# Kernel optimization log

Hardware: AMD Instinct MI355X
Metric: run time of the kernel (lower is better)

The kernel has to match this reference:

```python
import jax, jax.numpy as jnp
import numpy as np

B, Q, K = 4, 512, 512
QUERY_SIZE = 512
KEY_SIZE = 512
NUM_HIDDENS = 256


def setup_inputs() -> dict:
    key = jax.random.key(0)
    k1, k2, k3, k4, k5 = jax.random.split(key, 5)
    queries = jax.random.normal(k1, (B, Q, 1, QUERY_SIZE), dtype=jnp.float32)
    keys = jax.random.normal(k2, (B, 1, K, KEY_SIZE), dtype=jnp.float32)
    # nn.Linear weights (bias=False); stored as (in, out) for einsum clarity
    W_q = jax.random.normal(k3, (QUERY_SIZE, NUM_HIDDENS), dtype=jnp.float32) * (1.0 / np.sqrt(QUERY_SIZE))
    W_k = jax.random.normal(k4, (KEY_SIZE, NUM_HIDDENS), dtype=jnp.float32) * (1.0 / np.sqrt(KEY_SIZE))
    w_v = jax.random.normal(k5, (NUM_HIDDENS,), dtype=jnp.float32) * (1.0 / np.sqrt(NUM_HIDDENS))
    return {"queries": queries, "keys": keys, "W_q": W_q, "W_k": W_k, "w_v": w_v}


def reference(queries, keys, W_q, W_k, w_v):
    # Project: queries (B,Q,1,Dq) -> (B,Q,1,H); keys (B,1,K,Dk) -> (B,1,K,H)
    q = jnp.einsum('bqod,dh->bqoh', queries, W_q)
    k = jnp.einsum('bokd,dh->bokh', keys, W_k)
    # Broadcast add -> (B,Q,K,H), tanh, reduce hidden via w_v -> (B,Q,K)
    features = jnp.tanh(q + k)
    scores = jnp.einsum('bqkh,h->bqk', features, w_v)
    return scores
```

## Files before the change

### kernel.cpp

```cpp
#include <hip/hip_runtime.h>
#include <hip/hip_bf16.h>

#define HH 256
#define DD 512
#define MM 2048
#define CSCALE 2.8853900817779268f

typedef __bf16 bf16x8 __attribute__((ext_vector_type(8)));
typedef float floatx4 __attribute__((ext_vector_type(4)));

__global__ __launch_bounds__(256) void prep_kernel(
    const float* __restrict__ Wq, const float* __restrict__ Wk,
    const float* __restrict__ wv,
    __bf16* __restrict__ Wt, float* __restrict__ wv2, float* __restrict__ sumWp)
{
  const int bx = blockIdx.x;
  if (bx < 256) {
    const int mat  = bx >> 7;
    const int tile = bx & 127;
    const int kt = tile & 15;
    const int nt = tile >> 4;
    const float* __restrict__ W = mat ? Wk : Wq;
    __bf16* __restrict__ Wo = Wt + (size_t)mat * HH * DD;
    __shared__ float lds[32][33];
    const int i = threadIdx.x >> 5;
    const int j = threadIdx.x & 31;
    const int k0 = kt * 32, n0 = nt * 32;
#pragma unroll
    for (int p = 0; p < 4; ++p)
      lds[i + p * 8][j] = W[(k0 + i + p * 8) * HH + n0 + j];
    __syncthreads();
#pragma unroll
    for (int p = 0; p < 4; ++p) {
      const int n = i + p * 8;
      Wo[(n0 + n) * DD + k0 + j] = (__bf16)(lds[j][n] * CSCALE);
    }
  } else {
    __shared__ float red[256];
    const int t = threadIdx.x;
    float w = wv[t];
    wv2[t] = -2.0f * w;
    red[t] = w;
    __syncthreads();
    for (int s = 128; s > 0; s >>= 1) {
      if (t < s) red[t] += red[t + s];
      __syncthreads();
    }
    if (t == 0) *sumWp = red[0];
  }
}

__global__ __launch_bounds__(256) void proj_kernel(
    const float* __restrict__ queries, const float* __restrict__ keys,
    const __bf16* __restrict__ Wt,
    __bf16* __restrict__ eqp, float* __restrict__ ekp)
{
  const int w    = threadIdx.x >> 6;
  const int lane = threadIdx.x & 63;
  const int quad = lane >> 4;
  const int r    = lane & 15;
  const bool is_k = (blockIdx.z != 0);
  const float* __restrict__ X = is_k ? keys : queries;
  const __bf16* __restrict__ Wb = Wt + (is_k ? (size_t)HH * DD : 0);

  const int m0 = blockIdx.x * 32 + (w >> 1) * 16;
  const int n0 = blockIdx.y * 64 + (w & 1) * 32;

  floatx4 acc0 = {0.f, 0.f, 0.f, 0.f};
  floatx4 acc1 = {0.f, 0.f, 0.f, 0.f};
  const float* arow = X + (size_t)(m0 + r) * DD + quad * 8;
  const __bf16* b0 = Wb + (size_t)(n0 + r) * DD + quad * 8;
  const __bf16* b1 = b0 + 16 * DD;

  for (int kk = 0; kk < DD; kk += 32) {
    float4 a0 = *(const float4*)(arow + kk);
    float4 a1 = *(const float4*)(arow + kk + 4);
    bf16x8 af;
    af[0] = (__bf16)a0.x; af[1] = (__bf16)a0.y;
    af[2] = (__bf16)a0.z; af[3] = (__bf16)a0.w;
    af[4] = (__bf16)a1.x; af[5] = (__bf16)a1.y;
    af[6] = (__bf16)a1.z; af[7] = (__bf16)a1.w;
    bf16x8 bf0 = *(const bf16x8*)(b0 + kk);
    bf16x8 bf1 = *(const bf16x8*)(b1 + kk);
    acc0 = __builtin_amdgcn_mfma_f32_16x16x32_bf16(af, bf0, acc0, 0, 0, 0);
    acc1 = __builtin_amdgcn_mfma_f32_16x16x32_bf16(af, bf1, acc1, 0, 0, 0);
  }

  const int mrow = m0 + quad * 4;
  if (!is_k) {
#pragma unroll
    for (int i = 0; i < 4; ++i) {
      eqp[(size_t)(mrow + i) * HH + n0 + r] =
          (__bf16)__builtin_amdgcn_exp2f(acc0[i]);
      eqp[(size_t)(mrow + i) * HH + n0 + 16 + r] =
          (__bf16)__builtin_amdgcn_exp2f(acc1[i]);
    }
  } else {
#pragma unroll
    for (int i = 0; i < 4; ++i) {
      int na = n0 + r, nb = n0 + 16 + r;
      ekp[((size_t)(na >> 2) * MM + (mrow + i)) * 4 + (na & 3)] =
          __builtin_amdgcn_exp2f(acc0[i]);
      ekp[((size_t)(nb >> 2) * MM + (mrow + i)) * 4 + (nb & 3)] =
          __builtin_amdgcn_exp2f(acc1[i]);
    }
  }
}

__global__ __launch_bounds__(256) void score_kernel(
    const __bf16* __restrict__ eqp, const float4* __restrict__ ekp,
    const float* __restrict__ wv2, const float* __restrict__ sumWp,
    float* __restrict__ out)
{
  const int t  = threadIdx.x;
  const int b  = blockIdx.z;
  const int k  = blockIdx.x * 256 + t;
  const int q0 = blockIdx.y * 2;
  const float sumW = *sumWp;

  const float4* __restrict__ kptr = ekp + (size_t)b * 512 + k;
  const unsigned* __restrict__ qrow0 =
      (const unsigned*)(eqp + (size_t)(b * 512 + q0) * HH);
  const unsigned* __restrict__ qrow1 =
      (const unsigned*)(eqp + (size_t)(b * 512 + q0 + 1) * HH);

  float acc0 = 0.f, acc1 = 0.f;

#pragma unroll 8
  for (int hq = 0; hq < 64; ++hq) {
    float4 ek = kptr[(size_t)hq * MM];
    float4 w4 = *(const float4*)(wv2 + hq * 4);
    unsigned pa0 = qrow0[hq * 2], pb0 = qrow0[hq * 2 + 1];
    unsigned pa1 = qrow1[hq * 2], pb1 = qrow1[hq * 2 + 1];
    float q00 = __uint_as_float(pa0 << 16);
    float q01 = __uint_as_float(pa0 & 0xffff0000u);
    float q02 = __uint_as_float(pb0 << 16);
    float q03 = __uint_as_float(pb0 & 0xffff0000u);
    float q10 = __uint_as_float(pa1 << 16);
    float q11 = __uint_as_float(pa1 & 0xffff0000u);
    float q12 = __uint_as_float(pb1 << 16);
    float q13 = __uint_as_float(pb1 & 0xffff0000u);
    acc0 = fmaf(w4.x, __builtin_amdgcn_rcpf(fmaf(q00, ek.x, 1.0f)), acc0);
    acc0 = fmaf(w4.y, __builtin_amdgcn_rcpf(fmaf(q01, ek.y, 1.0f)), acc0);
    acc0 = fmaf(w4.z, __builtin_amdgcn_rcpf(fmaf(q02, ek.z, 1.0f)), acc0);
    acc0 = fmaf(w4.w, __builtin_amdgcn_rcpf(fmaf(q03, ek.w, 1.0f)), acc0);
    acc1 = fmaf(w4.x, __builtin_amdgcn_rcpf(fmaf(q10, ek.x, 1.0f)), acc1);
    acc1 = fmaf(w4.y, __builtin_amdgcn_rcpf(fmaf(q11, ek.y, 1.0f)), acc1);
    acc1 = fmaf(w4.z, __builtin_amdgcn_rcpf(fmaf(q12, ek.z, 1.0f)), acc1);
    acc1 = fmaf(w4.w, __builtin_amdgcn_rcpf(fmaf(q13, ek.w, 1.0f)), acc1);
  }

  const size_t obase = ((size_t)b * 512 + q0) * 512 + blockIdx.x * 256 + t;
  out[obase]       = sumW + acc0;
  out[obase + 512] = sumW + acc1;
}

extern "C" void kernel_launch(void* const* d_in, const int* in_sizes, int n_in,
                              void* d_out, int out_size, void* d_ws, size_t ws_size,
                              hipStream_t stream) {
  (void)in_sizes; (void)n_in; (void)out_size; (void)ws_size;
  const float* queries = (const float*)d_in[0];
  const float* keys    = (const float*)d_in[1];
  const float* Wq      = (const float*)d_in[2];
  const float* Wk      = (const float*)d_in[3];
  const float* wv      = (const float*)d_in[4];
  float* out = (float*)d_out;

  char* ws = (char*)d_ws;
  __bf16* Wt    = (__bf16*)ws;
  float*  wv2   = (float*)(ws + (512 << 10));
  float*  sumWp = (float*)(ws + (513 << 10));
  __bf16* eqp   = (__bf16*)(ws + (1 << 20));
  float*  ekp   = (float*)(ws + (2 << 20));

  prep_kernel<<<dim3(257), 256, 0, stream>>>(Wq, Wk, wv, Wt, wv2, sumWp);
  proj_kernel<<<dim3(64, 4, 2), 256, 0, stream>>>(queries, keys, Wt, eqp, ekp);
  score_kernel<<<dim3(2, 256, 4), 256, 0, stream>>>(
      eqp, (const float4*)ekp, wv2, sumWp, out);
}
```

Before: 115.5 us.

## Pair hidden units to halve reciprocals and use packed fp32 math in scoring

The score kernel now combines two hidden units over a common denominator: w0/(1+P0) + w1/(1+P1) becomes (w0(1+P1) + w1(1+P0)) / ((1+P0)(1+P1)). That needs only one reciprocal per pair instead of two. The arithmetic runs on two-wide float vectors so the compiler can emit packed fp32 FMAs. The query exponentials are also stored as fp32 instead of bf16, which removes the bit-unpacking work but doubles that buffer's traffic. The risk is overflow: the product of two large exponentials can reach inf, and inf*0 combinations could produce NaN.

```diff
diff --git a/kernel.cpp b/kernel.cpp
--- a/kernel.cpp
+++ b/kernel.cpp
@@ -8,11 +8,13 @@
 
 typedef __bf16 bf16x8 __attribute__((ext_vector_type(8)));
 typedef float floatx4 __attribute__((ext_vector_type(4)));
+typedef float float2v __attribute__((ext_vector_type(2)));
 
 __global__ __launch_bounds__(256) void prep_kernel(
     const float* __restrict__ Wq, const float* __restrict__ Wk,
     const float* __restrict__ wv,
-    __bf16* __restrict__ Wt, float* __restrict__ wv2, float* __restrict__ sumWp)
+    __bf16* __restrict__ Wt, float* __restrict__ wv2,
+    float2v* __restrict__ wsum2, float* __restrict__ sumWp)
 {
   const int bx = blockIdx.x;
   if (bx < 256) {
@@ -40,6 +42,12 @@
     const int t = threadIdx.x;
     float w = wv[t];
     wv2[t] = -2.0f * w;
+    if (t < 64) {
+      float2v ws;
+      ws.x = -2.0f * (wv[4 * t + 0] + wv[4 * t + 2]);
+      ws.y = -2.0f * (wv[4 * t + 1] + wv[4 * t + 3]);
+      wsum2[t] = ws;
+    }
     red[t] = w;
     __syncthreads();
     for (int s = 128; s > 0; s >>= 1) {
@@ -53,7 +61,7 @@
 __global__ __launch_bounds__(256) void proj_kernel(
     const float* __restrict__ queries, const float* __restrict__ keys,
     const __bf16* __restrict__ Wt,
-    __bf16* __restrict__ eqp, float* __restrict__ ekp)
+    float* __restrict__ eqp, float* __restrict__ ekp)
 {
   const int w    = threadIdx.x >> 6;
   const int lane = threadIdx.x & 63;
@@ -91,9 +99,9 @@
 #pragma unroll
     for (int i = 0; i < 4; ++i) {
       eqp[(size_t)(mrow + i) * HH + n0 + r] =
-          (__bf16)__builtin_amdgcn_exp2f(acc0[i]);
+          __builtin_amdgcn_exp2f(acc0[i]);
       eqp[(size_t)(mrow + i) * HH + n0 + 16 + r] =
-          (__bf16)__builtin_amdgcn_exp2f(acc1[i]);
+          __builtin_amdgcn_exp2f(acc1[i]);
     }
   } else {
 #pragma unroll
@@ -107,10 +115,25 @@
   }
 }
 
+__device__ __forceinline__ float2v pair_step(
+    float2v eq01, float2v eq23, float2v ek01, float2v ek23,
+    float2v Wlo, float2v Whi, float2v Ws, float2v acc)
+{
+  float2v Pl = eq01 * ek01;
+  float2v Ph = eq23 * ek23;
+  float2v s  = Pl + Ph;
+  float2v tt = __builtin_elementwise_fma(Pl, Ph, s);
+  float2v d  = tt + (float2v){1.0f, 1.0f};
+  float2v n  = __builtin_elementwise_fma(Wlo, Ph, Ws);
+  n          = __builtin_elementwise_fma(Whi, Pl, n);
+  float2v r  = {__builtin_amdgcn_rcpf(d.x), __builtin_amdgcn_rcpf(d.y)};
+  return __builtin_elementwise_fma(n, r, acc);
+}
+
 __global__ __launch_bounds__(256) void score_kernel(
-    const __bf16* __restrict__ eqp, const float4* __restrict__ ekp,
-    const float* __restrict__ wv2, const float* __restrict__ sumWp,
-    float* __restrict__ out)
+    const float* __restrict__ eqp, const float4* __restrict__ ekp,
+    const float4* __restrict__ wv2, const float2v* __restrict__ wsum2,
+    const float* __restrict__ sumWp, float* __restrict__ out)
 {
   const int t  = threadIdx.x;
   const int b  = blockIdx.z;
@@ -119,40 +142,30 @@
   const float sumW = *sumWp;
 
   const float4* __restrict__ kptr = ekp + (size_t)b * 512 + k;
-  const unsigned* __restrict__ qrow0 =
-      (const unsigned*)(eqp + (size_t)(b * 512 + q0) * HH);
-  const unsigned* __restrict__ qrow1 =
-      (const unsigned*)(eqp + (size_t)(b * 512 + q0 + 1) * HH);
+  const float2v* __restrict__ qrow0 =
+      (const float2v*)(eqp + (size_t)(b * 512 + q0) * HH);
+  const float2v* __restrict__ qrow1 = qrow0 + HH / 2;
 
-  float acc0 = 0.f, acc1 = 0.f;
+  float2v acc0 = {0.f, 0.f}, acc1 = {0.f, 0.f};
 
 #pragma unroll 8
   for (int hq = 0; hq < 64; ++hq) {
-    float4 ek = kptr[(size_t)hq * MM];
-    float4 w4 = *(const float4*)(wv2 + hq * 4);
-    unsigned pa0 = qrow0[hq * 2], pb0 = qrow0[hq * 2 + 1];
-    unsigned pa1 = qrow1[hq * 2], pb1 = qrow1[hq * 2 + 1];
-    float q00 = __uint_as_float(pa0 << 16);
-    float q01 = __uint_as_float(pa0 & 0xffff0000u);
-    float q02 = __uint_as_float(pb0 << 16);
-    float q03 = __uint_as_float(pb0 & 0xffff0000u);
-    float q10 = __uint_as_float(pa1 << 16);
-    float q11 = __uint_as_float(pa1 & 0xffff0000u);
-    float q12 = __uint_as_float(pb1 << 16);
-    float q13 = __uint_as_float(pb1 & 0xffff0000u);
-    acc0 = fmaf(w4.x, __builtin_amdgcn_rcpf(fmaf(q00, ek.x, 1.0f)), acc0);
-    acc0 = fmaf(w4.y, __builtin_amdgcn_rcpf(fmaf(q01, ek.y, 1.0f)), acc0);
-    acc0 = fmaf(w4.z, __builtin_amdgcn_rcpf(fmaf(q02, ek.z, 1.0f)), acc0);
-    acc0 = fmaf(w4.w, __builtin_amdgcn_rcpf(fmaf(q03, ek.w, 1.0f)), acc0);
-    acc1 = fmaf(w4.x, __builtin_amdgcn_rcpf(fmaf(q10, ek.x, 1.0f)), acc1);
-    acc1 = fmaf(w4.y, __builtin_amdgcn_rcpf(fmaf(q11, ek.y, 1.0f)), acc1);
-    acc1 = fmaf(w4.z, __builtin_amdgcn_rcpf(fmaf(q12, ek.z, 1.0f)), acc1);
-    acc1 = fmaf(w4.w, __builtin_amdgcn_rcpf(fmaf(q13, ek.w, 1.0f)), acc1);
+    float4 ek4 = kptr[(size_t)hq * MM];
+    float2v ek01 = {ek4.x, ek4.y};
+    float2v ek23 = {ek4.z, ek4.w};
+    float4 w4 = wv2[hq];
+    float2v Wlo = {w4.x, w4.y};
+    float2v Whi = {w4.z, w4.w};
+    float2v Ws  = wsum2[hq];
+    float2v eq01a = qrow0[hq * 2], eq23a = qrow0[hq * 2 + 1];
+    float2v eq01b = qrow1[hq * 2], eq23b = qrow1[hq * 2 + 1];
+    acc0 = pair_step(eq01a, eq23a, ek01, ek23, Wlo, Whi, Ws, acc0);
+    acc1 = pair_step(eq01b, eq23b, ek01, ek23, Wlo, Whi, Ws, acc1);
   }
 
   const size_t obase = ((size_t)b * 512 + q0) * 512 + blockIdx.x * 256 + t;
-  out[obase]       = sumW + acc0;
-  out[obase + 512] = sumW + acc1;
+  out[obase]       = sumW + acc0.x + acc0.y;
+  out[obase + 512] = sumW + acc1.x + acc1.y;
 }
 
 extern "C" void kernel_launch(void* const* d_in, const int* in_sizes, int n_in,
@@ -167,14 +180,15 @@
   float* out = (float*)d_out;
 
   char* ws = (char*)d_ws;
-  __bf16* Wt    = (__bf16*)ws;
-  float*  wv2   = (float*)(ws + (512 << 10));
-  float*  sumWp = (float*)(ws + (513 << 10));
-  __bf16* eqp   = (__bf16*)(ws + (1 << 20));
-  float*  ekp   = (float*)(ws + (2 << 20));
+  __bf16*  Wt    = (__bf16*)ws;
+  float*   wv2   = (float*)(ws + (512 << 10));
+  float2v* wsum2 = (float2v*)(ws + (513 << 10));
+  float*   sumWp = (float*)(ws + (514 << 10));
+  float*   eqp   = (float*)(ws + (1 << 20));
+  float*   ekp   = (float*)(ws + (3 << 20));
 
-  prep_kernel<<<dim3(257), 256, 0, stream>>>(Wq, Wk, wv, Wt, wv2, sumWp);
+  prep_kernel<<<dim3(257), 256, 0, stream>>>(Wq, Wk, wv, Wt, wv2, wsum2, sumWp);
   proj_kernel<<<dim3(64, 4, 2), 256, 0, stream>>>(queries, keys, Wt, eqp, ekp);
   score_kernel<<<dim3(2, 256, 4), 256, 0, stream>>>(
-      eqp, (const float4*)ekp, wv2, sumWp, out);
+      eqp, (const float4*)ekp, (const float4*)wv2, wsum2, sumWp, out);
 }
```

Result: slower. 120.3 us (+4.2%).
